# Optimization experiments

Measured on AMD Instinct MI355X. Metric: run time of the kernel, lower is better.

The kernel has to match this reference:

```python
import jax, jax.numpy as jnp
import numpy as np

B, S, F, H, D = 32, 512, 32, 8, 300   # batch, seq, n_features, hidden_dim, n_dim_model
FH = min(D, F)                        # flattened GRN hidden = min(n_dim_model, n_features)


def _p(key, shape, scale=0.05):
    return (jax.random.normal(key, shape) * scale).astype(jnp.float32)


def setup_inputs() -> dict:
    key = jax.random.key(0)
    ks = jax.random.split(key, 16)
    return {
        "x": jax.random.normal(ks[0], (B, S, F), dtype=jnp.float32),
        "pre_w": _p(ks[1], (F, H)), "pre_b": _p(ks[2], (F, H)),
        "sg_fc1_w": _p(ks[3], (F, H, H)), "sg_fc1_b": _p(ks[4], (F, H)),
        "sg_fc2_w": _p(ks[5], (F, H, D)), "sg_fc2_b": _p(ks[6], (F, D)),
        "sg_gate_w": _p(ks[7], (F, D, 2 * D)), "sg_gate_b": _p(ks[8], (F, 2 * D)),
        "sg_ln_g": jnp.ones((F, D), jnp.float32), "sg_ln_b": jnp.zeros((F, D), jnp.float32),
        "fl_fc1_w": _p(ks[9], (F * H, FH)), "fl_fc1_b": _p(ks[10], (FH,)),
        "fl_fc2_w": _p(ks[11], (FH, F)), "fl_fc2_b": _p(ks[12], (F,)),
        "fl_gate_w": _p(ks[13], (F, 2 * F)), "fl_gate_b": _p(ks[14], (2 * F,)),
        "fl_ln_g": jnp.ones((F,), jnp.float32), "fl_ln_b": jnp.zeros((F,), jnp.float32),
    }


def _interp_last(x, out_dim):
    # torch F.interpolate(mode='linear', align_corners=True) along the last axis
    in_dim = x.shape[-1]
    pos = jnp.arange(out_dim) * ((in_dim - 1) / (out_dim - 1))
    lo = jnp.floor(pos).astype(jnp.int32)
    hi = jnp.minimum(lo + 1, in_dim - 1)
    w = (pos - lo.astype(pos.dtype)).astype(x.dtype)
    return x[..., lo] * (1 - w) + x[..., hi] * w


def _layer_norm(x, g, b, eps=1e-5):
    m = jnp.mean(x, axis=-1, keepdims=True)
    v = jnp.var(x, axis=-1, keepdims=True)
    return (x - m) * jax.lax.rsqrt(v + eps) * g + b


def _forward(x, pre_w, pre_b, sg_fc1_w, sg_fc1_b, sg_fc2_w, sg_fc2_b,
             sg_gate_w, sg_gate_b, sg_ln_g, sg_ln_b,
             fl_fc1_w, fl_fc1_b, fl_fc2_w, fl_fc2_b, fl_gate_w, fl_gate_b,
             fl_ln_g, fl_ln_b):
    # per-feature prescaler: Linear(1, H) for each of F features, batched
    pre = x[..., None] * pre_w + pre_b                                   # [B,S,F,H]

    # per-feature GRN (H -> H -> D), batched over the feature axis f
    h = jax.nn.elu(jnp.einsum('bsfh,fhk->bsfk', pre, sg_fc1_w) + sg_fc1_b)
    h = jnp.einsum('bsfk,fkd->bsfd', h, sg_fc2_w) + sg_fc2_b             # [B,S,F,D]
    g = jnp.einsum('bsfd,fdp->bsfp', h, sg_gate_w) + sg_gate_b           # [B,S,F,2D]
    glu = g[..., :D] * jax.nn.sigmoid(g[..., D:])
    residual = _interp_last(pre, D)                                      # H -> D interpolate projection
    outputs = _layer_norm(glu + residual, sg_ln_g, sg_ln_b)              # [B,S,F,D]

    # flattened GRN on concatenated prescaler outputs (F*H -> FH -> F)
    flat = pre.reshape(pre.shape[0], pre.shape[1], F * H)                # matches torch.cat order
    fh = jax.nn.elu(flat @ fl_fc1_w + fl_fc1_b)
    fh = fh @ fl_fc2_w + fl_fc2_b                                        # [B,S,F]
    fg = fh @ fl_gate_w + fl_gate_b                                      # [B,S,2F]
    fglu = fg[..., :F] * jax.nn.sigmoid(fg[..., F:])
    wlogits = _layer_norm(fglu + _interp_last(flat, F), fl_ln_g, fl_ln_b)
    w = jax.nn.softmax(wlogits, axis=-1)                                 # [B,S,F]

    out = jnp.einsum('bsfd,bsf->bsd', outputs, w)                        # softmax-weighted sum over features
    return out, w[..., None, :]                                          # weights unsqueezed at dim -2


def reference(x, pre_w, pre_b, sg_fc1_w, sg_fc1_b, sg_fc2_w, sg_fc2_b,
              sg_gate_w, sg_gate_b, sg_ln_g, sg_ln_b,
              fl_fc1_w, fl_fc1_b, fl_fc2_w, fl_fc2_b, fl_gate_w, fl_gate_b,
              fl_ln_g, fl_ln_b):
    return _forward(x, pre_w, pre_b, sg_fc1_w, sg_fc1_b, sg_fc2_w, sg_fc2_b,
                    sg_gate_w, sg_gate_b, sg_ln_g, sg_ln_b,
                    fl_fc1_w, fl_fc1_b, fl_fc2_w, fl_fc2_b, fl_gate_w, fl_gate_b,
                    fl_ln_g, fl_ln_b)
```

## Files before the change

kernel.cpp:

```cpp
#include <hip/hip_runtime.h>
#include <hip/hip_bf16.h>
#include <hip/hip_fp16.h>

#define NB 32
#define NS 512
#define NF 32
#define NH 8
#define ND 300
#define NTOK (NB*NS)
#define TPW 8
#define WPB 2
#define TPB (TPW*WPB)

#define L2E 1.4426950408889634f

#define NFD (NF*ND)
#define PA_OFF 0
#define PB_OFF (NFD*4)
#define CC_OFF (NFD*8)

using bf16 = __hip_bfloat16;
typedef float v2f __attribute__((ext_vector_type(2)));
typedef _Float16 h2 __attribute__((ext_vector_type(2)));

__device__ __forceinline__ h2 ash2(unsigned u){
    union { unsigned u; h2 h; } c; c.u = u; return c.h;
}
__device__ __forceinline__ float fdot2_(unsigned a, unsigned b, float acc){
    return __builtin_amdgcn_fdot2(ash2(a), ash2(b), acc, false);
}
__device__ __forceinline__ float h_lo(unsigned u){
    return (float)ash2(u).x;
}
__device__ __forceinline__ float h_hi(unsigned u){
    return (float)ash2(u).y;
}

__device__ __forceinline__ float rcpf_(float x){ return __builtin_amdgcn_rcpf(x); }
__device__ __forceinline__ float rsqf_(float x){ return __builtin_amdgcn_rsqf(x); }
__device__ __forceinline__ float sigm(float x){ return rcpf_(1.0f + __expf(-x)); }
__device__ __forceinline__ float sigm2(float x){ return rcpf_(1.0f + __builtin_amdgcn_exp2f(-x)); }
__device__ __forceinline__ float eluf(float x){ return x > 0.0f ? x : __expf(x) - 1.0f; }

__device__ __forceinline__ v2f fma2(v2f a, v2f b, v2f c){
    return __builtin_elementwise_fma(a, b, c);
}
__device__ __forceinline__ v2f fma2s(float s, v2f b, v2f c){
    return __builtin_elementwise_fma((v2f){s, s}, b, c);
}

template<int BF16>
__device__ __forceinline__ float ldf(const void* p, size_t i){
    if (BF16) return __bfloat162float(((const bf16*)p)[i]);
    return ((const float*)p)[i];
}
template<int BF16>
__device__ __forceinline__ void stf(void* p, size_t i, float v){
    if (BF16) ((bf16*)p)[i] = __float2bfloat16(v);
    else      ((float*)p)[i] = v;
}

__device__ __forceinline__ bool is_bf16(const void* ones){
    return *(const unsigned*)ones == 0x3F803F80u;
}

__device__ __forceinline__ unsigned pack_h(float a, float b){
    __half ha = __float2half(a), hb = __float2half(b);
    return (unsigned)*(unsigned short*)&ha | ((unsigned)*(unsigned short*)&hb << 16);
}

template<int CTRL>
__device__ __forceinline__ float dppadd(float v){
    return v + __int_as_float(__builtin_amdgcn_update_dpp(
        0, __float_as_int(v), CTRL, 0xF, 0xF, true));
}
template<int CTRL>
__device__ __forceinline__ float dppmax(float v){
    return fmaxf(v, __int_as_float(__builtin_amdgcn_update_dpp(
        __float_as_int(v), __float_as_int(v), CTRL, 0xF, 0xF, false)));
}
__device__ __forceinline__ float rlane(float v, int l){
    return __int_as_float(__builtin_amdgcn_readlane(__float_as_int(v), l));
}
__device__ __forceinline__ float wsum64(float v){
    v = dppadd<0x111>(v); v = dppadd<0x112>(v); v = dppadd<0x114>(v); v = dppadd<0x118>(v);
    v = dppadd<0x142>(v); v = dppadd<0x143>(v);
    return rlane(v, 63);
}
__device__ __forceinline__ float rsum32(float v){
    v = dppadd<0x111>(v); v = dppadd<0x112>(v); v = dppadd<0x114>(v); v = dppadd<0x118>(v);
    return rlane(v, 15) + rlane(v, 31);
}
__device__ __forceinline__ float rmax32(float v){
    v = dppmax<0x111>(v); v = dppmax<0x112>(v); v = dppmax<0x114>(v); v = dppmax<0x118>(v);
    return fmaxf(rlane(v, 15), rlane(v, 31));
}

template<int BF16>
__device__ void precompute_body(const void* __restrict__ W2, const void* __restrict__ b2,
                                const void* __restrict__ Wg, const void* __restrict__ bg,
                                const void* __restrict__ sg_g, const void* __restrict__ sg_b,
                                const void* __restrict__ pre_w, const void* __restrict__ pre_b,
                                unsigned* __restrict__ Crow,
                                float* __restrict__ w2t, float* __restrict__ b2s,
                                float (*part)[64][18])
{
    const int tid  = threadIdx.x;
    const int lane = tid & 63;
    const int wv   = tid >> 6;
    const int f    = blockIdx.x & 31;
    const int c    = blockIdx.x >> 5;
    const int d    = c * 64 + lane;
    const int dc   = d < 299 ? d : 299;

    for (int idx = tid; idx < 2400; idx += 512) {
        int m = idx >> 3, k = idx & 7;
        w2t[idx] = ldf<BF16>(W2, (size_t)f * 2400 + (size_t)k * 300 + m);
    }
    if (tid < 300) b2s[tid] = ldf<BF16>(b2, (size_t)f * 300 + tid);
    __syncthreads();

    v2f aA01 = {0,0}, aA23 = {0,0}, aA45 = {0,0}, aA67 = {0,0};
    v2f aB01 = {0,0}, aB23 = {0,0}, aB45 = {0,0}, aB67 = {0,0};
    float bAa = 0.f, bBa = 0.f;

    const int m0 = (wv * 300) >> 3;
    const int m1 = ((wv + 1) * 300) >> 3;
    const size_t WgF = (size_t)f * 180000 + dc;
    #pragma unroll 4
    for (int m = m0; m < m1; ++m) {
        float wa = ldf<BF16>(Wg, WgF + (size_t)m * 600);
        float wb = ldf<BF16>(Wg, WgF + (size_t)m * 600 + 300);
        float4 wk0 = *(const float4*)(w2t + m * 8);
        float4 wk1 = *(const float4*)(w2t + m * 8 + 4);
        aA01 = fma2s(wa, (v2f){wk0.x, wk0.y}, aA01);
        aA23 = fma2s(wa, (v2f){wk0.z, wk0.w}, aA23);
        aA45 = fma2s(wa, (v2f){wk1.x, wk1.y}, aA45);
        aA67 = fma2s(wa, (v2f){wk1.z, wk1.w}, aA67);
        aB01 = fma2s(wb, (v2f){wk0.x, wk0.y}, aB01);
        aB23 = fma2s(wb, (v2f){wk0.z, wk0.w}, aB23);
        aB45 = fma2s(wb, (v2f){wk1.x, wk1.y}, aB45);
        aB67 = fma2s(wb, (v2f){wk1.z, wk1.w}, aB67);
        float b2v = b2s[m];
        bAa += b2v * wa;
        bBa += b2v * wb;
    }

    {
        float* p = part[wv][lane];
        p[0]  = aA01.x; p[1]  = aA01.y; p[2]  = aA23.x; p[3]  = aA23.y;
        p[4]  = aA45.x; p[5]  = aA45.y; p[6]  = aA67.x; p[7]  = aA67.y;
        p[8]  = aB01.x; p[9]  = aB01.y; p[10] = aB23.x; p[11] = aB23.y;
        p[12] = aB45.x; p[13] = aB45.y; p[14] = aB67.x; p[15] = aB67.y;
        p[16] = bAa;    p[17] = bBa;
    }
    __syncthreads();

    if (tid < 64 && d < 300) {
        float s[18];
        #pragma unroll
        for (int v = 0; v < 18; ++v) {
            float t0 = part[0][lane][v] + part[1][lane][v];
            float t1 = part[2][lane][v] + part[3][lane][v];
            float t2 = part[4][lane][v] + part[5][lane][v];
            float t3 = part[6][lane][v] + part[7][lane][v];
            s[v] = (t0 + t1) + (t2 + t3);
        }
        unsigned dwA[4], dwB[4];
        #pragma unroll
        for (int j = 0; j < 4; ++j) {
            dwA[j] = pack_h(s[2 * j],     s[2 * j + 1]);
            dwB[j] = pack_h(s[8 + 2 * j] * L2E, s[9 + 2 * j] * L2E);
        }
        unsigned bA = __float_as_uint(s[16] + ldf<BF16>(bg, (size_t)f * 600 + d));
        unsigned bB = __float_as_uint((s[17] + ldf<BF16>(bg, (size_t)f * 600 + d + 300)) * L2E);
        float lgf = ldf<BF16>(sg_g, (size_t)f * 300 + d);
        float lbf = ldf<BF16>(sg_b, (size_t)f * 300 + d);

        float pos = (float)d * (7.0f / 299.0f);
        int lo = (int)floorf(pos); lo = lo < 0 ? 0 : (lo > 6 ? 6 : lo);
        float fr = pos - (float)lo;
        float pwl = ldf<BF16>(pre_w, (size_t)f * 8 + lo);
        float pwh = ldf<BF16>(pre_w, (size_t)f * 8 + lo + 1);
        float pbl = ldf<BF16>(pre_b, (size_t)f * 8 + lo);
        float pbh = ldf<BF16>(pre_b, (size_t)f * 8 + lo + 1);
        float rwf = pwl + fr * (pwh - pwl);
        float rbf = pbl + fr * (pbh - pbl);

        const size_t fd = (size_t)f * ND + d;
        *(uint4*)(Crow + PA_OFF + fd * 4) = make_uint4(dwA[0], dwA[1], dwA[2], dwA[3]);
        *(uint4*)(Crow + PB_OFF + fd * 4) = make_uint4(dwB[0], dwB[1], dwB[2], dwB[3]);
        *(uint4*)(Crow + CC_OFF + fd * 4) =
            make_uint4(bA, bB, pack_h(lgf, lbf), pack_h(rwf, rbf));
    }
}

__global__ void precompute_kernel(const void* __restrict__ W2, const void* __restrict__ b2,
                                  const void* __restrict__ Wg, const void* __restrict__ bg,
                                  const void* __restrict__ sg_g, const void* __restrict__ sg_b,
                                  const void* __restrict__ pre_w, const void* __restrict__ pre_b,
                                  unsigned* __restrict__ Crow)
{
    __shared__ float w2t[2400];
    __shared__ float b2s[300];
    __shared__ float part[8][64][18];
    if (is_bf16(sg_g))
        precompute_body<1>(W2, b2, Wg, bg, sg_g, sg_b, pre_w, pre_b, Crow, w2t, b2s, part);
    else
        precompute_body<0>(W2, b2, Wg, bg, sg_g, sg_b, pre_w, pre_b, Crow, w2t, b2s, part);
}

template<int BF16>
__device__ void vsn_body(const void* __restrict__ x,
                         const void* __restrict__ pre_w, const void* __restrict__ pre_b,
                         const void* __restrict__ W1,    const void* __restrict__ b1,
                         const void* __restrict__ fl1w,  const void* __restrict__ fl1b,
                         const void* __restrict__ fl2w,  const void* __restrict__ fl2b,
                         const void* __restrict__ flgw,  const void* __restrict__ flgb,
                         const void* __restrict__ flng,  const void* __restrict__ flnb,
                         const unsigned* __restrict__ Crow,
                         void* __restrict__ d_out, float* preS_, unsigned* hS_)
{
    void* outMain = d_out;
    void* outW    = (char*)d_out + (size_t)NTOK * ND * (BF16 ? 2 : 4);

    const int tid  = threadIdx.x;
    const int wave = tid >> 6;
    const int lane = tid & 63;
    const int tokBase = blockIdx.x * TPB + wave * TPW;

    float*    myPre = preS_ + wave * (TPW * 256);
    unsigned* myH   = hS_   + wave * (TPW * 128);

    float xr0, xr1, xr2, xr3;
    {
        const int tx = lane & 7, fo = lane >> 3;
        const size_t bx = (size_t)(tokBase + tx) * NF + fo;
        xr0 = ldf<BF16>(x, bx);
        xr1 = ldf<BF16>(x, bx + 8);
        xr2 = ldf<BF16>(x, bx + 16);
        xr3 = ldf<BF16>(x, bx + 24);
    }

    {
        float pw[4], pb[4];
        #pragma unroll
        for (int q = 0; q < 4; ++q) {
            pw[q] = ldf<BF16>(pre_w, 4 * lane + q);
            pb[q] = ldf<BF16>(pre_b, 4 * lane + q);
        }
        const int fidx = lane >> 1;
        #pragma unroll
        for (int t = 0; t < TPW; ++t) {
            float xv = ldf<BF16>(x, (size_t)(tokBase + t) * NF + fidx);
            float4 v;
            v.x = xv * pw[0] + pb[0];
            v.y = xv * pw[1] + pb[1];
            v.z = xv * pw[2] + pb[2];
            v.w = xv * pw[3] + pb[3];
            *(float4*)(&myPre[t * 256 + 4 * lane]) = v;
        }
    }

    {
        const int f  = lane >> 1;
        const int kh = (lane & 1) * 4;
        float w1r[8][4], b1r[4];
        #pragma unroll
        for (int m = 0; m < 8; ++m)
            #pragma unroll
            for (int q = 0; q < 4; ++q)
                w1r[m][q] = ldf<BF16>(W1, (size_t)(f * 8 + m) * 8 + kh + q);
        #pragma unroll
        for (int q = 0; q < 4; ++q) b1r[q] = ldf<BF16>(b1, f * 8 + kh + q);

        #pragma unroll
        for (int t = 0; t < TPW; ++t) {
            float pr[8];
            float4 pA = *(const float4*)(&myPre[t * 256 + f * 8]);
            float4 pB = *(const float4*)(&myPre[t * 256 + f * 8 + 4]);
            pr[0]=pA.x; pr[1]=pA.y; pr[2]=pA.z; pr[3]=pA.w;
            pr[4]=pB.x; pr[5]=pB.y; pr[6]=pB.z; pr[7]=pB.w;
            float a[4] = {b1r[0], b1r[1], b1r[2], b1r[3]};
            #pragma unroll
            for (int m = 0; m < 8; ++m)
                #pragma unroll
                for (int q = 0; q < 4; ++q)
                    a[q] += pr[m] * w1r[m][q];
            uint2 hp;
            hp.x = pack_h(eluf(a[0]), eluf(a[1]));
            hp.y = pack_h(eluf(a[2]), eluf(a[3]));
            *(uint2*)(&myH[t * 128 + 2 * lane]) = hp;
        }
    }

    const int jj = lane & 31;
    const int hB = lane >> 5;
    float wreg[TPW];
    {
        float f1b = (hB == 0) ? ldf<BF16>(fl1b, jj) : 0.0f;
        v2f p1v[TPW / 2];
        #pragma unroll
        for (int g = 0; g < TPW / 2; ++g) p1v[g] = (v2f){f1b, f1b};
        for (int kg = 0; kg < 32; ++kg) {
            const int kk = hB * 128 + kg * 4;
            float4 pr[TPW];
            #pragma unroll
            for (int t = 0; t < TPW; ++t)
                pr[t] = *(const float4*)(&myPre[t * 256 + kk]);
            float w0 = ldf<BF16>(fl1w, (size_t)(kk + 0) * 32 + jj);
            float w1 = ldf<BF16>(fl1w, (size_t)(kk + 1) * 32 + jj);
            float w2 = ldf<BF16>(fl1w, (size_t)(kk + 2) * 32 + jj);
            float w3 = ldf<BF16>(fl1w, (size_t)(kk + 3) * 32 + jj);
            #pragma unroll
            for (int g = 0; g < TPW / 2; ++g) {
                p1v[g] = fma2((v2f){pr[2*g].x, pr[2*g+1].x}, (v2f){w0, w0}, p1v[g]);
                p1v[g] = fma2((v2f){pr[2*g].y, pr[2*g+1].y}, (v2f){w1, w1}, p1v[g]);
                p1v[g] = fma2((v2f){pr[2*g].z, pr[2*g+1].z}, (v2f){w2, w2}, p1v[g]);
                p1v[g] = fma2((v2f){pr[2*g].w, pr[2*g+1].w}, (v2f){w3, w3}, p1v[g]);
            }
        }
        float fhv[TPW];
        #pragma unroll
        for (int t = 0; t < TPW; ++t) {
            float p1 = (t & 1) ? p1v[t >> 1].y : p1v[t >> 1].x;
            fhv[t] = eluf(p1 + __shfl_xor(p1, 32));
        }

        float p2[TPW];
        float f2b = ldf<BF16>(fl2b, jj);
        #pragma unroll
        for (int t = 0; t < TPW; ++t) p2[t] = f2b;
        #pragma unroll
        for (int k = 0; k < 32; ++k) {
            float wv = ldf<BF16>(fl2w, k * 32 + jj);
            #pragma unroll
            for (int t = 0; t < TPW; ++t) p2[t] += rlane(fhv[t], k) * wv;
        }
        float p3[TPW];
        float fgbv = ldf<BF16>(flgb, lane);
        #pragma unroll
        for (int t = 0; t < TPW; ++t) p3[t] = fgbv;
        #pragma unroll
        for (int k = 0; k < 32; ++k) {
            float wv = ldf<BF16>(flgw, k * 64 + lane);
            #pragma unroll
            for (int t = 0; t < TPW; ++t) p3[t] += rlane(p2[t], k) * wv;
        }

        float lng = ldf<BF16>(flng, jj), lnb = ldf<BF16>(flnb, jj);
        float posB = (float)jj * (255.0f / 31.0f);
        int loB = (int)floorf(posB); loB = loB < 0 ? 0 : (loB > 254 ? 254 : loB);
        float frB = posB - (float)loB;

        #pragma unroll
        for (int t = 0; t < TPW; ++t) {
            float fgA  = __shfl(p3[t], jj);
            float fgB  = __shfl(p3[t], jj + 32);
            float fglu = fgA * sigm(fgB);
            float pl = myPre[t * 256 + loB];
            float ph = myPre[t * 256 + loB + 1];
            float tv = fglu + pl + frB * (ph - pl);
            float S1 = rsum32(tv);
            float S2 = rsum32(tv * tv);
            float mean = S1 * (1.0f / 32.0f);
            float var  = fmaxf(S2 * (1.0f / 32.0f) - mean * mean, 0.0f);
            float rs   = rsqf_(var + 1e-5f);
            float wl   = (tv - mean) * rs * lng + lnb;
            float mx   = rmax32(wl);
            float e    = __expf(wl - mx);
            float ss   = rsum32(e);
            float wv   = e * rcpf_(ss);
            wreg[t] = wv;
            if (lane < 32) stf<BF16>(outW, (size_t)(tokBase + t) * NF + lane, wv);
        }
    }

    float acc[TPW][5];
    #pragma unroll
    for (int t = 0; t < TPW; ++t)
        #pragma unroll
        for (int i = 0; i < 5; ++i) acc[t][i] = 0.0f;

    for (int f = 0; f < NF; ++f) {
        uint4 cpA[5], cpB[5];
        float bcA[5], bcB[5];
        unsigned lglb[5], rwrb[5];
        #pragma unroll
        for (int i = 0; i < 5; ++i) {
            int d = i * 64 + lane;
            int dcl = d < ND ? d : ND - 1;
            const size_t fd = (size_t)f * ND + dcl;
            cpA[i] = *(const uint4*)(Crow + PA_OFF + fd * 4);
            cpB[i] = *(const uint4*)(Crow + PB_OFF + fd * 4);
            uint4 c2 = *(const uint4*)(Crow + CC_OFF + fd * 4);
            bcA[i]  = __uint_as_float(c2.x);
            bcB[i]  = __uint_as_float(c2.y);
            lglb[i] = c2.z;
            rwrb[i] = c2.w;
        }

        float xq = (f < 8) ? xr0 : (f < 16) ? xr1 : (f < 24) ? xr2 : xr3;
        const int fl3 = (f & 7) << 3;

        #pragma unroll
        for (int t = 0; t < TPW; ++t) {
            uint4 hp = *(const uint4*)(&myH[t * 128 + f * 4]);
            float xv = rlane(xq, fl3 | t);

            float tt[5], a1 = 0.f, a2 = 0.f;
            #pragma unroll
            for (int i = 0; i < 5; ++i) {
                float gx = bcA[i], gy = bcB[i];
                gx = fdot2_(hp.x, cpA[i].x, gx);
                gx = fdot2_(hp.y, cpA[i].y, gx);
                gx = fdot2_(hp.z, cpA[i].z, gx);
                gx = fdot2_(hp.w, cpA[i].w, gx);
                gy = fdot2_(hp.x, cpB[i].x, gy);
                gy = fdot2_(hp.y, cpB[i].y, gy);
                gy = fdot2_(hp.z, cpB[i].z, gy);
                gy = fdot2_(hp.w, cpB[i].w, gy);
                float tv = fmaf(xv, h_lo(rwrb[i]), h_hi(rwrb[i])) + gx * sigm2(gy);
                if (i == 4) tv = (lane < (ND - 256)) ? tv : 0.0f;
                tt[i] = tv; a1 += tv; a2 = fmaf(tv, tv, a2);
            }

            float S1 = wsum64(a1);
            float S2 = wsum64(a2);
            float mean = S1 * (1.0f / 300.0f);
            float var  = fmaxf(S2 * (1.0f / 300.0f) - mean * mean, 0.0f);
            float rs   = rsqf_(var + 1e-5f);
            float wf   = rlane(wreg[t], f);
            float c1v  = wf * rs;
            float c2v  = -c1v * mean;
            #pragma unroll
            for (int i = 0; i < 4; ++i)
                acc[t][i] = fmaf(h_lo(lglb[i]), fmaf(c1v, tt[i], c2v),
                                 fmaf(wf, h_hi(lglb[i]), acc[t][i]));
            if (lane < (ND - 256))
                acc[t][4] = fmaf(h_lo(lglb[4]), fmaf(c1v, tt[4], c2v),
                                 fmaf(wf, h_hi(lglb[4]), acc[t][4]));
        }
    }

    #pragma unroll
    for (int t = 0; t < TPW; ++t) {
        const size_t tok = (size_t)tokBase + t;
        #pragma unroll
        for (int i = 0; i < 4; ++i)
            stf<BF16>(outMain, tok * ND + i * 64 + lane, acc[t][i]);
        if (lane < (ND - 256))
            stf<BF16>(outMain, tok * ND + 256 + lane, acc[t][4]);
    }
}

__launch_bounds__(128)
__global__ void vsn_main(const void* __restrict__ x,
                         const void* __restrict__ pre_w, const void* __restrict__ pre_b,
                         const void* __restrict__ W1,    const void* __restrict__ b1,
                         const void* __restrict__ fl1w,  const void* __restrict__ fl1b,
                         const void* __restrict__ fl2w,  const void* __restrict__ fl2b,
                         const void* __restrict__ flgw,  const void* __restrict__ flgb,
                         const void* __restrict__ flng,  const void* __restrict__ flnb,
                         const unsigned* __restrict__ Crow, void* __restrict__ d_out)
{
    __shared__ float    preS_[WPB * TPW * 256];
    __shared__ unsigned hS_[WPB * TPW * 128];
    if (is_bf16(flng))
        vsn_body<1>(x, pre_w, pre_b, W1, b1, fl1w, fl1b, fl2w, fl2b,
                    flgw, flgb, flng, flnb, Crow, d_out, preS_, hS_);
    else
        vsn_body<0>(x, pre_w, pre_b, W1, b1, fl1w, fl1b, fl2w, fl2b,
                    flgw, flgb, flng, flnb, Crow, d_out, preS_, hS_);
}

extern "C" void kernel_launch(void* const* d_in, const int* in_sizes, int n_in,
                              void* d_out, int out_size, void* d_ws, size_t ws_size,
                              hipStream_t stream)
{
    const void* x     = d_in[0];
    const void* pre_w = d_in[1];
    const void* pre_b = d_in[2];
    const void* W1    = d_in[3];
    const void* b1    = d_in[4];
    const void* W2    = d_in[5];
    const void* b2    = d_in[6];
    const void* Wg    = d_in[7];
    const void* bg    = d_in[8];
    const void* sg_g  = d_in[9];
    const void* sg_b  = d_in[10];
    const void* fl1w  = d_in[11];
    const void* fl1b  = d_in[12];
    const void* fl2w  = d_in[13];
    const void* fl2b  = d_in[14];
    const void* flgw  = d_in[15];
    const void* flgb  = d_in[16];
    const void* flng  = d_in[17];
    const void* flnb  = d_in[18];

    unsigned* Crow = (unsigned*)d_ws;

    precompute_kernel<<<160, 512, 0, stream>>>(W2, b2, Wg, bg, sg_g, sg_b,
                                               pre_w, pre_b, Crow);

    vsn_main<<<NTOK / TPB, 128, 0, stream>>>(x, pre_w, pre_b, W1, b1,
        fl1w, fl1b, fl2w, fl2b, flgw, flgb, flng, flnb, Crow, d_out);
}
```

Baseline: 280.2 us.

## Pack biases, x values and softmax weights into fp16 pairs to cut register pressure

Gate biases are stored as an fp16 pair in one dword of the per-feature constant record. The per-token x values and softmax weights are held as packed fp16 pairs instead of separate floats, and are unpacked through readlane plus a shift. Together with a launch-bounds minimum-blocks hint, this is meant to reduce VGPR use and raise occupancy. In exchange it lowers the precision of x, the softmax weights and the gate biases to fp16, and adds unpack instructions to the inner loop.

```diff
diff --git a/kernel.cpp b/kernel.cpp
--- a/kernel.cpp
+++ b/kernel.cpp
@@ -81,6 +81,9 @@
 }
 __device__ __forceinline__ float rlane(float v, int l){
     return __int_as_float(__builtin_amdgcn_readlane(__float_as_int(v), l));
+}
+__device__ __forceinline__ unsigned rlaneu(unsigned v, int l){
+    return (unsigned)__builtin_amdgcn_readlane((int)v, l);
 }
 __device__ __forceinline__ float wsum64(float v){
     v = dppadd<0x111>(v); v = dppadd<0x112>(v); v = dppadd<0x114>(v); v = dppadd<0x118>(v);
@@ -172,8 +175,8 @@
             dwA[j] = pack_h(s[2 * j],     s[2 * j + 1]);
             dwB[j] = pack_h(s[8 + 2 * j] * L2E, s[9 + 2 * j] * L2E);
         }
-        unsigned bA = __float_as_uint(s[16] + ldf<BF16>(bg, (size_t)f * 600 + d));
-        unsigned bB = __float_as_uint((s[17] + ldf<BF16>(bg, (size_t)f * 600 + d + 300)) * L2E);
+        float bAf = s[16] + ldf<BF16>(bg, (size_t)f * 600 + d);
+        float bBf = (s[17] + ldf<BF16>(bg, (size_t)f * 600 + d + 300)) * L2E;
         float lgf = ldf<BF16>(sg_g, (size_t)f * 300 + d);
         float lbf = ldf<BF16>(sg_b, (size_t)f * 300 + d);
 
@@ -191,7 +194,7 @@
         *(uint4*)(Crow + PA_OFF + fd * 4) = make_uint4(dwA[0], dwA[1], dwA[2], dwA[3]);
         *(uint4*)(Crow + PB_OFF + fd * 4) = make_uint4(dwB[0], dwB[1], dwB[2], dwB[3]);
         *(uint4*)(Crow + CC_OFF + fd * 4) =
-            make_uint4(bA, bB, pack_h(lgf, lbf), pack_h(rwf, rbf));
+            make_uint4(pack_h(bAf, bBf), pack_h(lgf, lbf), pack_h(rwf, rbf), 0u);
     }
 }
 
@@ -232,14 +235,12 @@
     float*    myPre = preS_ + wave * (TPW * 256);
     unsigned* myH   = hS_   + wave * (TPW * 128);
 
-    float xr0, xr1, xr2, xr3;
+    unsigned xp0, xp1;
     {
         const int tx = lane & 7, fo = lane >> 3;
         const size_t bx = (size_t)(tokBase + tx) * NF + fo;
-        xr0 = ldf<BF16>(x, bx);
-        xr1 = ldf<BF16>(x, bx + 8);
-        xr2 = ldf<BF16>(x, bx + 16);
-        xr3 = ldf<BF16>(x, bx + 24);
+        xp0 = pack_h(ldf<BF16>(x, bx),      ldf<BF16>(x, bx + 8));
+        xp1 = pack_h(ldf<BF16>(x, bx + 16), ldf<BF16>(x, bx + 24));
     }
 
     {
@@ -296,7 +297,7 @@
 
     const int jj = lane & 31;
     const int hB = lane >> 5;
-    float wreg[TPW];
+    unsigned wp[TPW / 2];
     {
         float f1b = (hB == 0) ? ldf<BF16>(fl1b, jj) : 0.0f;
         v2f p1v[TPW / 2];
@@ -353,6 +354,7 @@
         int loB = (int)floorf(posB); loB = loB < 0 ? 0 : (loB > 254 ? 254 : loB);
         float frB = posB - (float)loB;
 
+        float wprev = 0.0f;
         #pragma unroll
         for (int t = 0; t < TPW; ++t) {
             float fgA  = __shfl(p3[t], jj);
@@ -371,7 +373,8 @@
             float e    = __expf(wl - mx);
             float ss   = rsum32(e);
             float wv   = e * rcpf_(ss);
-            wreg[t] = wv;
+            if (t & 1) wp[t >> 1] = pack_h(wprev, wv);
+            else       wprev = wv;
             if (lane < 32) stf<BF16>(outW, (size_t)(tokBase + t) * NF + lane, wv);
         }
     }
@@ -384,8 +387,7 @@
 
     for (int f = 0; f < NF; ++f) {
         uint4 cpA[5], cpB[5];
-        float bcA[5], bcB[5];
-        unsigned lglb[5], rwrb[5];
+        unsigned bcp[5], lglb[5], rwrb[5];
         #pragma unroll
         for (int i = 0; i < 5; ++i) {
             int d = i * 64 + lane;
@@ -394,24 +396,26 @@
             cpA[i] = *(const uint4*)(Crow + PA_OFF + fd * 4);
             cpB[i] = *(const uint4*)(Crow + PB_OFF + fd * 4);
             uint4 c2 = *(const uint4*)(Crow + CC_OFF + fd * 4);
-            bcA[i]  = __uint_as_float(c2.x);
-            bcB[i]  = __uint_as_float(c2.y);
-            lglb[i] = c2.z;
-            rwrb[i] = c2.w;
-        }
-
-        float xq = (f < 8) ? xr0 : (f < 16) ? xr1 : (f < 24) ? xr2 : xr3;
+            bcp[i]  = c2.x;
+            lglb[i] = c2.y;
+            rwrb[i] = c2.z;
+        }
+
+        unsigned xq = (f < 16) ? xp0 : xp1;
+        const unsigned xsh = (unsigned)((f & 8) << 1);
         const int fl3 = (f & 7) << 3;
 
         #pragma unroll
         for (int t = 0; t < TPW; ++t) {
             uint4 hp = *(const uint4*)(&myH[t * 128 + f * 4]);
-            float xv = rlane(xq, fl3 | t);
+            float xv = h_lo(rlaneu(xq, fl3 | t) >> xsh);
+            unsigned wdw = rlaneu(wp[t >> 1], f);
+            float wf = (t & 1) ? h_hi(wdw) : h_lo(wdw);
 
             float tt[5], a1 = 0.f, a2 = 0.f;
             #pragma unroll
             for (int i = 0; i < 5; ++i) {
-                float gx = bcA[i], gy = bcB[i];
+                float gx = h_lo(bcp[i]), gy = h_hi(bcp[i]);
                 gx = fdot2_(hp.x, cpA[i].x, gx);
                 gx = fdot2_(hp.y, cpA[i].y, gx);
                 gx = fdot2_(hp.z, cpA[i].z, gx);
@@ -430,7 +434,6 @@
             float mean = S1 * (1.0f / 300.0f);
             float var  = fmaxf(S2 * (1.0f / 300.0f) - mean * mean, 0.0f);
             float rs   = rsqf_(var + 1e-5f);
-            float wf   = rlane(wreg[t], f);
             float c1v  = wf * rs;
             float c2v  = -c1v * mean;
             #pragma unroll
@@ -454,7 +457,7 @@
     }
 }
 
-__launch_bounds__(128)
+__launch_bounds__(128, 2)
 __global__ void vsn_main(const void* __restrict__ x,
                          const void* __restrict__ pre_w, const void* __restrict__ pre_b,
                          const void* __restrict__ W1,    const void* __restrict__ b1,
```

After: 270.5 us. -3.5%, faster.
